# Kernel tuning notes

Measured on AMD Instinct MI355X. Metric: run time of the kernel, lower is better.

Reference implementation:

```python
import jax, jax.numpy as jnp
import numpy as np

N = 50000
IN_CH = 128
HEADS = 4
OUT_CH = 16
HID = HEADS * OUT_CH  # 64
E = 800000
B_EXP = 2.0
EPS = 1e-06
LN_EPS = 1e-05

def _l2norm(v, axis):
    n = jnp.sqrt(jnp.sum(v * v, axis=axis, keepdims=True))
    return v / jnp.maximum(n, 1e-12)  # matches F.normalize eps

def setup_inputs() -> dict:
    key = jax.random.key(0)
    k1, k2, k3, k4 = jax.random.split(key, 4)
    x = jax.random.normal(k1, (N, IN_CH), dtype=jnp.float32)
    edge_index = jax.random.randint(k2, (2, E), 0, N, dtype=jnp.int64)
    # lin: xavier_uniform over [HID, IN_CH]
    bound = float(np.sqrt(6.0 / (HID + IN_CH)))
    lin_w = jax.random.uniform(k3, (HID, IN_CH), dtype=jnp.float32, minval=-bound, maxval=bound)
    bcos_w = jax.random.normal(k4, (HID, HID), dtype=jnp.float32) * (1.0 / np.sqrt(HID))
    ln_gamma = jnp.ones((HID,), dtype=jnp.float32)
    ln_beta = jnp.zeros((HID,), dtype=jnp.float32)
    return {"x": x, "edge_index": edge_index, "lin_w": lin_w,
            "bcos_w": bcos_w, "ln_gamma": ln_gamma, "ln_beta": ln_beta}

def reference(x, edge_index, lin_w, bcos_w, ln_gamma, ln_beta):
    row, col = edge_index[0], edge_index[1]
    h = (x @ lin_w.T).reshape(N, HEADS, OUT_CH)          # [N,H,D]
    h_norm = _l2norm(h, axis=2)
    # per-edge cosine between source (col) and target (row) node features
    cos = jnp.sum(h_norm[col] * h_norm[row], axis=2)     # [E,H]
    cos = jnp.clip(cos, EPS, 1.0)
    scale = cos ** (B_EXP - 1.0)                         # [E,H]
    messages = h[col] * scale[:, :, None]                # [E,H,D]
    # scatter-add messages to target nodes
    out = jax.ops.segment_sum(messages.reshape(E, HID), row, num_segments=N)  # [N,HID]
    # BcosLinearNoBias
    lin = out @ bcos_w.T
    o_n = _l2norm(out, axis=1)
    w_n = _l2norm(bcos_w, axis=1)
    cos2 = jnp.clip(o_n @ w_n.T, EPS, 1.0)
    out_bcos = lin * cos2 ** (B_EXP - 1.0)
    # LayerNorm
    mu = jnp.mean(out_bcos, axis=-1, keepdims=True)
    var = jnp.mean((out_bcos - mu) ** 2, axis=-1, keepdims=True)
    out_norm = (out_bcos - mu) / jnp.sqrt(var + LN_EPS) * ln_gamma + ln_beta
    # dropout is identity in eval mode
    return out_norm
```

## Files before the change

### kernel.cpp

```cpp
#include <hip/hip_runtime.h>
#include <math.h>

#define N_NODES 50000
#define IN_CH   128
#define HEADS   4
#define HID     64
#define NEDGE   800000
#define EPS     1e-6f
#define LN_EPS  1e-5f
#define NT4     (N_NODES / 4)
#define PAD     48

#define DPP_ADD_F(p, ctrl) \
    p += __int_as_float(__builtin_amdgcn_update_dpp(0, __float_as_int(p), ctrl, 0xF, 0xF, true))
#define REDUCE16_DPP(p) { DPP_ADD_F(p,0xB1); DPP_ADD_F(p,0x4E); \
                          DPP_ADD_F(p,0x141); DPP_ADD_F(p,0x140); }
#define REDUCE4_DPP(p)  { DPP_ADD_F(p,0xB1); DPP_ADD_F(p,0x4E); }
#define REDUCE64(p) { REDUCE16_DPP(p); p += __shfl_xor(p,16); p += __shfl_xor(p,32); }

__global__ __launch_bounds__(512) void h_kernel(const float* __restrict__ x,
                                                const float* __restrict__ lin_w,
                                                float* __restrict__ h,
                                                float* __restrict__ inv_hn,
                                                const int* __restrict__ ei,
                                                int* __restrict__ deg,
                                                int* __restrict__ csr_col) {
    __shared__ float4 wt[32 * 65];
    __shared__ float4 xsl[8][128];

    const float4* w4g = (const float4*)lin_w;
    for (int i = threadIdx.x; i < HID * (IN_CH / 4); i += 512) {
        int c = i >> 5, k4 = i & 31;
        wt[k4 * 65 + c] = w4g[i];
    }

    int wave = threadIdx.x >> 6;
    int lane = threadIdx.x & 63;
    int g = blockIdx.x * 8 + wave;
    bool have_g = (g < NT4);

    const float4* xp = (const float4*)x;
    float4 v0, v1;
    if (have_g) {
        v0 = xp[(size_t)g * 128 + lane];
        v1 = xp[(size_t)g * 128 + 64 + lane];
    }

    int t = blockIdx.x * 512 + threadIdx.x;
    bool have_e = (t < NEDGE / 4);
    int4 r, c;
    if (have_e) {
        r = ((const int4*)ei)[t];
        c = ((const int4*)(ei + NEDGE))[t];
    }

    __syncthreads();

    int k0, k1, k2, k3;
    if (have_e) {
        k0 = atomicAdd(&deg[r.x], 1);
        k1 = atomicAdd(&deg[r.y], 1);
        k2 = atomicAdd(&deg[r.z], 1);
        k3 = atomicAdd(&deg[r.w], 1);
    }

    if (have_g) {
        float4* myxs = xsl[wave];
        myxs[lane]      = v0;
        myxs[64 + lane] = v1;

        float a0 = 0.f, a1 = 0.f, a2 = 0.f, a3 = 0.f;
#pragma unroll 2
        for (int k4 = 0; k4 < IN_CH / 4; ++k4) {
            float4 wv = wt[k4 * 65 + lane];
            float4 x0 = myxs[0 * 32 + k4];
            float4 x1 = myxs[1 * 32 + k4];
            float4 x2 = myxs[2 * 32 + k4];
            float4 x3 = myxs[3 * 32 + k4];
            a0 += wv.x * x0.x + wv.y * x0.y + wv.z * x0.z + wv.w * x0.w;
            a1 += wv.x * x1.x + wv.y * x1.y + wv.z * x1.z + wv.w * x1.w;
            a2 += wv.x * x2.x + wv.y * x2.y + wv.z * x2.z + wv.w * x2.w;
            a3 += wv.x * x3.x + wv.y * x3.y + wv.z * x3.z + wv.w * x3.w;
        }

        int n0 = g * 4;
        float accs[4] = {a0, a1, a2, a3};
#pragma unroll
        for (int j = 0; j < 4; ++j) {
            int node = n0 + j;
            h[node * HID + lane] = accs[j];
            float ss = accs[j] * accs[j];
            REDUCE16_DPP(ss);
            if ((lane & 15) == 0)
                inv_hn[node * HEADS + (lane >> 4)] = 1.0f / fmaxf(sqrtf(ss), 1e-12f);
        }
    }

    if (have_e) {
        if (k0 < PAD) __builtin_nontemporal_store(c.x, &csr_col[r.x * PAD + k0]);
        if (k1 < PAD) __builtin_nontemporal_store(c.y, &csr_col[r.y * PAD + k1]);
        if (k2 < PAD) __builtin_nontemporal_store(c.z, &csr_col[r.z * PAD + k2]);
        if (k3 < PAD) __builtin_nontemporal_store(c.w, &csr_col[r.w * PAD + k3]);
    }
}

__global__ __launch_bounds__(256, 4) void gather_final(const int* __restrict__ deg,
                                                       const int* __restrict__ csr_col,
                                                       const float* __restrict__ h,
                                                       const float* __restrict__ inv_hn,
                                                       const float* __restrict__ bcos_w,
                                                       const float* __restrict__ gamma,
                                                       const float* __restrict__ beta,
                                                       float* __restrict__ y) {
    __shared__ float4 wt4[16][65];
    __shared__ float rowbuf[4][HID];
    __shared__ float ivw[HID], gm[HID], bt[HID];

    for (int i = threadIdx.x; i < HID * (HID / 4); i += 256) {
        int j = i >> 4, k4 = i & 15;
        wt4[k4][j] = ((const float4*)bcos_w)[i];
    }
    if (threadIdx.x < HID) {
        gm[threadIdx.x] = gamma[threadIdx.x];
        bt[threadIdx.x] = beta[threadIdx.x];
    }
    __syncthreads();
    if (threadIdx.x < HID) {
        float ss = 0.f;
#pragma unroll
        for (int k4 = 0; k4 < 16; ++k4) {
            float4 q = wt4[k4][threadIdx.x];
            ss += q.x * q.x + q.y * q.y + q.z * q.z + q.w * q.w;
        }
        ivw[threadIdx.x] = 1.0f / fmaxf(sqrtf(ss), 1e-12f);
    }
    __syncthreads();

    int grp    = threadIdx.x >> 6;
    int lane   = threadIdx.x & 63;
    int e_slot = lane >> 4;
    int ch4    = lane & 15;
    int hd     = ch4 >> 2;
    int head   = lane >> 4;

    const float4* h4 = (const float4*)h;

    for (int g = blockIdx.x; g < N_NODES / 4; g += gridDim.x) {
        int node = g * 4 + grp;
        float4 hq  = h4[node * 16 + ch4];
        float  ihr = inv_hn[node * HEADS + hd];
        float4 hrs4 = make_float4(hq.x * ihr, hq.y * ihr, hq.z * ihr, hq.w * ihr);
        int dg    = __builtin_amdgcn_readfirstlane(min(deg[node], PAD));
        int start = node * PAD;

        float4 acc = make_float4(0.f, 0.f, 0.f, 0.f);
#pragma unroll 1
        for (int bb = 0; bb < dg; bb += 16) {
            int   cc[4];
            float4 hh[4];
            float ii[4];
#pragma unroll
            for (int s = 0; s < 4; ++s) {
                int e = bb + s * 4 + e_slot;
                int ix = (e < dg) ? e : dg - 1;
                cc[s] = csr_col[start + ix];
            }
#pragma unroll
            for (int s = 0; s < 4; ++s) hh[s] = h4[cc[s] * 16 + ch4];
#pragma unroll
            for (int s = 0; s < 4; ++s) ii[s] = inv_hn[cc[s] * HEADS + hd];
#pragma unroll
            for (int s = 0; s < 4; ++s) {
                float p = hh[s].x * hrs4.x + hh[s].y * hrs4.y
                        + hh[s].z * hrs4.z + hh[s].w * hrs4.w;
                REDUCE4_DPP(p);
                float sc = fminf(fmaxf(p * ii[s], EPS), 1.0f);
                int e = bb + s * 4 + e_slot;
                sc = (e < dg) ? sc : 0.0f;
                acc.x = fmaf(hh[s].x, sc, acc.x);
                acc.y = fmaf(hh[s].y, sc, acc.y);
                acc.z = fmaf(hh[s].z, sc, acc.z);
                acc.w = fmaf(hh[s].w, sc, acc.w);
            }
        }
        acc.x += __shfl_xor(acc.x, 16); acc.x += __shfl_xor(acc.x, 32);
        acc.y += __shfl_xor(acc.y, 16); acc.y += __shfl_xor(acc.y, 32);
        acc.z += __shfl_xor(acc.z, 16); acc.z += __shfl_xor(acc.z, 32);
        acc.w += __shfl_xor(acc.w, 16); acc.w += __shfl_xor(acc.w, 32);

        if (lane < 16) ((float4*)rowbuf[grp])[ch4] = acc;
        float o = rowbuf[grp][lane];

        float ss = o * o;
        REDUCE64(ss);
        float inv_no = 1.0f / fmaxf(sqrtf(ss), 1e-12f);

        const float4* rb4 = (const float4*)rowbuf[grp];
        float lin = 0.f;
#pragma unroll
        for (int k4 = 0; k4 < 16; ++k4) {
            float4 a  = rb4[k4];
            float4 wv = wt4[k4][lane];
            lin += a.x * wv.x + a.y * wv.y + a.z * wv.z + a.w * wv.w;
        }

        float c2v = lin * inv_no * ivw[lane];
        c2v = fminf(fmaxf(c2v, EPS), 1.0f);
        float ob = lin * c2v;

        float mu = ob;
        REDUCE64(mu);
        mu *= (1.0f / 64.0f);
        float d = ob - mu;
        float var = d * d;
        REDUCE64(var);
        var *= (1.0f / 64.0f);
        float r = rsqrtf(var + LN_EPS);
        y[node * HID + lane] = d * r * gm[lane] + bt[lane];
        (void)head;
    }
}

extern "C" void kernel_launch(void* const* d_in, const int* in_sizes, int n_in,
                              void* d_out, int out_size, void* d_ws, size_t ws_size,
                              hipStream_t stream) {
    const float* x      = (const float*)d_in[0];
    const int*   ei     = (const int*)d_in[1];
    const float* lin_w  = (const float*)d_in[2];
    const float* bcos_w = (const float*)d_in[3];
    const float* gamma  = (const float*)d_in[4];
    const float* beta   = (const float*)d_in[5];
    float*       y      = (float*)d_out;

    float* h       = (float*)d_ws;
    float* inv_hn  = h + (size_t)N_NODES * HID;
    int*   deg     = (int*)(inv_hn + (size_t)N_NODES * HEADS);
    int*   csr_col = deg + N_NODES;

    const int H_BLOCKS = (NT4 + 7) / 8;

    hipMemsetAsync(deg, 0, N_NODES * sizeof(int), stream);

    h_kernel<<<H_BLOCKS, 512, 0, stream>>>(x, lin_w, h, inv_hn, ei, deg, csr_col);

    gather_final<<<2048, 256, 0, stream>>>(deg, csr_col, h, inv_hn,
                                           bcos_w, gamma, beta, y);
}
```

Baseline: 122.1 us.

## Compute node projection with fp16 MFMA 16x16x32 tiles instead of FP32 FMA loops

Replaces the scalar FP32 LDS-staged projection x @ lin_w^T with per-wave 16-node tiles computed by MFMA f16 instructions. x and the weights are converted to half precision in registers, and the weights are read directly from global/L2 instead of an LDS transpose. This removes the shared-memory staging and block-wide barrier, and the block size shrinks to 256 threads. The cost is reduced input precision in h, which could affect accuracy, and repeated weight loads per wave.

```diff
diff --git a/kernel.cpp b/kernel.cpp
--- a/kernel.cpp
+++ b/kernel.cpp
@@ -8,8 +8,11 @@
 #define NEDGE   800000
 #define EPS     1e-6f
 #define LN_EPS  1e-5f
-#define NT4     (N_NODES / 4)
 #define PAD     48
+#define MTILES  (N_NODES / 16)
+
+typedef __attribute__((ext_vector_type(8))) _Float16 f16x8;
+typedef __attribute__((ext_vector_type(4))) float    f32x4;
 
 #define DPP_ADD_F(p, ctrl) \
     p += __int_as_float(__builtin_amdgcn_update_dpp(0, __float_as_int(p), ctrl, 0xF, 0xF, true))
@@ -18,44 +21,23 @@
 #define REDUCE4_DPP(p)  { DPP_ADD_F(p,0xB1); DPP_ADD_F(p,0x4E); }
 #define REDUCE64(p) { REDUCE16_DPP(p); p += __shfl_xor(p,16); p += __shfl_xor(p,32); }
 
-__global__ __launch_bounds__(512) void h_kernel(const float* __restrict__ x,
-                                                const float* __restrict__ lin_w,
-                                                float* __restrict__ h,
-                                                float* __restrict__ inv_hn,
-                                                const int* __restrict__ ei,
-                                                int* __restrict__ deg,
-                                                int* __restrict__ csr_col) {
-    __shared__ float4 wt[32 * 65];
-    __shared__ float4 xsl[8][128];
-
-    const float4* w4g = (const float4*)lin_w;
-    for (int i = threadIdx.x; i < HID * (IN_CH / 4); i += 512) {
-        int c = i >> 5, k4 = i & 31;
-        wt[k4 * 65 + c] = w4g[i];
-    }
-
+__global__ __launch_bounds__(256, 4) void h_kernel(const float* __restrict__ x,
+                                                   const float* __restrict__ lin_w,
+                                                   float* __restrict__ h,
+                                                   float* __restrict__ inv_hn,
+                                                   const int* __restrict__ ei,
+                                                   int* __restrict__ deg,
+                                                   int* __restrict__ csr_col) {
+    int lane = threadIdx.x & 63;
     int wave = threadIdx.x >> 6;
-    int lane = threadIdx.x & 63;
-    int g = blockIdx.x * 8 + wave;
-    bool have_g = (g < NT4);
-
-    const float4* xp = (const float4*)x;
-    float4 v0, v1;
-    if (have_g) {
-        v0 = xp[(size_t)g * 128 + lane];
-        v1 = xp[(size_t)g * 128 + 64 + lane];
-    }
-
-    int t = blockIdx.x * 512 + threadIdx.x;
+
+    int t = blockIdx.x * 256 + threadIdx.x;
     bool have_e = (t < NEDGE / 4);
     int4 r, c;
     if (have_e) {
         r = ((const int4*)ei)[t];
         c = ((const int4*)(ei + NEDGE))[t];
     }
-
-    __syncthreads();
-
     int k0, k1, k2, k3;
     if (have_e) {
         k0 = atomicAdd(&deg[r.x], 1);
@@ -64,35 +46,55 @@
         k3 = atomicAdd(&deg[r.w], 1);
     }
 
-    if (have_g) {
-        float4* myxs = xsl[wave];
-        myxs[lane]      = v0;
-        myxs[64 + lane] = v1;
-
-        float a0 = 0.f, a1 = 0.f, a2 = 0.f, a3 = 0.f;
-#pragma unroll 2
-        for (int k4 = 0; k4 < IN_CH / 4; ++k4) {
-            float4 wv = wt[k4 * 65 + lane];
-            float4 x0 = myxs[0 * 32 + k4];
-            float4 x1 = myxs[1 * 32 + k4];
-            float4 x2 = myxs[2 * 32 + k4];
-            float4 x3 = myxs[3 * 32 + k4];
-            a0 += wv.x * x0.x + wv.y * x0.y + wv.z * x0.z + wv.w * x0.w;
-            a1 += wv.x * x1.x + wv.y * x1.y + wv.z * x1.z + wv.w * x1.w;
-            a2 += wv.x * x2.x + wv.y * x2.y + wv.z * x2.z + wv.w * x2.w;
-            a3 += wv.x * x3.x + wv.y * x3.y + wv.z * x3.z + wv.w * x3.w;
-        }
-
-        int n0 = g * 4;
-        float accs[4] = {a0, a1, a2, a3};
-#pragma unroll
-        for (int j = 0; j < 4; ++j) {
-            int node = n0 + j;
-            h[node * HID + lane] = accs[j];
-            float ss = accs[j] * accs[j];
-            REDUCE16_DPP(ss);
-            if ((lane & 15) == 0)
-                inv_hn[node * HEADS + (lane >> 4)] = 1.0f / fmaxf(sqrtf(ss), 1e-12f);
+    int mt = blockIdx.x * 4 + wave;
+    if (mt < MTILES) {
+        int node0 = mt * 16;
+        int mrow  = lane & 15;
+        int kg    = lane >> 4;
+        const float4* xp = (const float4*)x;
+        const float4* w4 = (const float4*)lin_w;
+
+        f16x8 A[4];
+#pragma unroll
+        for (int s = 0; s < 4; ++s) {
+            float4 u0 = xp[(node0 + mrow) * 32 + s * 8 + kg * 2];
+            float4 u1 = xp[(node0 + mrow) * 32 + s * 8 + kg * 2 + 1];
+            f16x8 a;
+            a[0] = (_Float16)u0.x; a[1] = (_Float16)u0.y;
+            a[2] = (_Float16)u0.z; a[3] = (_Float16)u0.w;
+            a[4] = (_Float16)u1.x; a[5] = (_Float16)u1.y;
+            a[6] = (_Float16)u1.z; a[7] = (_Float16)u1.w;
+            A[s] = a;
+        }
+
+#pragma unroll
+        for (int nt = 0; nt < 4; ++nt) {
+            f32x4 C = {0.f, 0.f, 0.f, 0.f};
+#pragma unroll
+            for (int s = 0; s < 4; ++s) {
+                int wrow = nt * 16 + mrow;
+                float4 u0 = w4[wrow * 32 + s * 8 + kg * 2];
+                float4 u1 = w4[wrow * 32 + s * 8 + kg * 2 + 1];
+                f16x8 b;
+                b[0] = (_Float16)u0.x; b[1] = (_Float16)u0.y;
+                b[2] = (_Float16)u0.z; b[3] = (_Float16)u0.w;
+                b[4] = (_Float16)u1.x; b[5] = (_Float16)u1.y;
+                b[6] = (_Float16)u1.z; b[7] = (_Float16)u1.w;
+                C = __builtin_amdgcn_mfma_f32_16x16x32_f16(A[s], b, C, 0, 0, 0);
+            }
+            float ss0 = C[0] * C[0], ss1 = C[1] * C[1];
+            float ss2 = C[2] * C[2], ss3 = C[3] * C[3];
+#pragma unroll
+            for (int rr = 0; rr < 4; ++rr)
+                h[(node0 + 4 * kg + rr) * HID + nt * 16 + mrow] = C[rr];
+            REDUCE16_DPP(ss0); REDUCE16_DPP(ss1);
+            REDUCE16_DPP(ss2); REDUCE16_DPP(ss3);
+            if (mrow == 0) {
+                inv_hn[(node0 + 4 * kg + 0) * HEADS + nt] = 1.0f / fmaxf(sqrtf(ss0), 1e-12f);
+                inv_hn[(node0 + 4 * kg + 1) * HEADS + nt] = 1.0f / fmaxf(sqrtf(ss1), 1e-12f);
+                inv_hn[(node0 + 4 * kg + 2) * HEADS + nt] = 1.0f / fmaxf(sqrtf(ss2), 1e-12f);
+                inv_hn[(node0 + 4 * kg + 3) * HEADS + nt] = 1.0f / fmaxf(sqrtf(ss3), 1e-12f);
+            }
         }
     }
 
@@ -141,7 +143,6 @@
     int e_slot = lane >> 4;
     int ch4    = lane & 15;
     int hd     = ch4 >> 2;
-    int head   = lane >> 4;
 
     const float4* h4 = (const float4*)h;
 
@@ -217,7 +218,6 @@
         var *= (1.0f / 64.0f);
         float r = rsqrtf(var + LN_EPS);
         y[node * HID + lane] = d * r * gm[lane] + bt[lane];
-        (void)head;
     }
 }
 
@@ -237,11 +237,11 @@
     int*   deg     = (int*)(inv_hn + (size_t)N_NODES * HEADS);
     int*   csr_col = deg + N_NODES;
 
-    const int H_BLOCKS = (NT4 + 7) / 8;
+    const int H_BLOCKS = (MTILES + 3) / 4;
 
     hipMemsetAsync(deg, 0, N_NODES * sizeof(int), stream);
 
-    h_kernel<<<H_BLOCKS, 512, 0, stream>>>(x, lin_w, h, inv_hn, ei, deg, csr_col);
+    h_kernel<<<H_BLOCKS, 256, 0, stream>>>(x, lin_w, h, inv_hn, ei, deg, csr_col);
 
     gather_final<<<2048, 256, 0, stream>>>(deg, csr_col, h, inv_hn,
                                            bcos_w, gamma, beta, y);
```

Result: slower. 126.2 us (+3.4%).
